# Optimization experiments

Measured on AMD Instinct MI355X. Metric: run time of the kernel, lower is better.

Reference implementation:

```python
import jax, jax.numpy as jnp
import numpy as np
import math

N_HEAD = 16

def _rope_tables(seq, dh, dtype):
    inv_freq = 1.0 / (10000.0 ** (jnp.arange(0, dh, 2, dtype=jnp.float32) / dh))
    angle = jnp.arange(seq, dtype=jnp.float32)[:, None] * inv_freq[None, :]  # [S, dh/2]
    sin = jnp.repeat(jnp.sin(angle), 2, axis=-1).astype(dtype)  # [S, dh]
    cos = jnp.repeat(jnp.cos(angle), 2, axis=-1).astype(dtype)
    return sin, cos

def _rotate_half(x):
    x_even = x[..., ::2]
    x_odd = x[..., 1::2]
    return jnp.stack([-x_odd, x_even], axis=-1).reshape(x.shape)

def _apply_rope(x, sin, cos):
    # x: [B, H, S, dh]; sin/cos: [S, dh]
    return x * cos[None, None] + _rotate_half(x) * sin[None, None]

def setup_inputs() -> dict:
    key = jax.random.key(0)
    ks = jax.random.split(key, 9)
    B, S, D = 2, 2048, 2048
    scale = 1.0 / math.sqrt(D)
    x = jax.random.normal(ks[0], (B, S, D), dtype=jnp.float32)
    wq = jax.random.normal(ks[1], (D, D), dtype=jnp.float32) * scale
    wk = jax.random.normal(ks[2], (D, D), dtype=jnp.float32) * scale
    wv = jax.random.normal(ks[3], (D, D), dtype=jnp.float32) * scale
    wo = jax.random.normal(ks[4], (D, D), dtype=jnp.float32) * scale
    bq = jnp.zeros((D,), jnp.float32)
    bk = jnp.zeros((D,), jnp.float32)
    bv = jnp.zeros((D,), jnp.float32)
    bo = jnp.zeros((D,), jnp.float32)
    # causal mask: True = masked (strict upper triangle)
    mask = jnp.triu(jnp.ones((S, S), dtype=bool), k=1)[None, None]  # [1,1,S,S]
    return {"x": x, "wq": wq, "bq": bq, "wk": wk, "bk": bk, "wv": wv, "bv": bv,
            "wo": wo, "bo": bo, "mask": mask}

def reference(x, wq, bq, wk, bk, wv, bv, wo, bo, mask):
    B, S, D = x.shape
    H = N_HEAD
    dh = D // H
    # projections (torch Linear: x @ W.T + b)
    q = (x @ wq.T + bq).reshape(B, S, H, dh).transpose(0, 2, 1, 3)  # [B,H,S,dh]
    k = (x @ wk.T + bk).reshape(B, S, H, dh).transpose(0, 2, 1, 3)
    v = (x @ wv.T + bv).reshape(B, S, H, dh).transpose(0, 2, 1, 3)
    sin, cos = _rope_tables(S, dh, x.dtype)
    q = _apply_rope(q, sin, cos)
    k = _apply_rope(k, sin, cos)
    scores = jnp.einsum('bhqd,bhkd->bhqk', q, k) / math.sqrt(dh)
    scores = jnp.where(mask, -jnp.inf, scores)
    attn = jax.nn.softmax(scores, axis=-1)
    attn = jnp.nan_to_num(attn, nan=0.0)
    out = jnp.einsum('bhqk,bhkd->bhqd', attn, v)  # [B,H,S,dh]
    out = out.transpose(0, 2, 1, 3).reshape(B, S, D)
    return out @ wo.T + bo
```

## Files before the change

### kernel.cpp

```cpp
#include <hip/hip_runtime.h>
#include <math.h>


typedef _Float16 half8 __attribute__((ext_vector_type(8)));
typedef _Float16 half4v __attribute__((ext_vector_type(4)));
typedef float f32x4 __attribute__((ext_vector_type(4)));

__device__ __forceinline__ void gl_lds16(const void* g, void* l) {
  __builtin_amdgcn_global_load_lds(
      (const __attribute__((address_space(1))) unsigned int*)g,
      (__attribute__((address_space(3))) unsigned int*)l, 16, 0, 0);
}

__global__ void cast_f32_f16(const float* __restrict__ src, _Float16* __restrict__ dst, int n4) {
  int i = blockIdx.x * blockDim.x + threadIdx.x;
  if (i >= n4) return;
  float4 v = reinterpret_cast<const float4*>(src)[i];
  half4v o;
  o[0] = (_Float16)v.x; o[1] = (_Float16)v.y; o[2] = (_Float16)v.z; o[3] = (_Float16)v.w;
  reinterpret_cast<half4v*>(dst)[i] = o;
}

__global__ void cast_w(const float* __restrict__ w0, const float* __restrict__ w1,
                       const float* __restrict__ w2, const float* __restrict__ w3,
                       _Float16* __restrict__ wdst) {
  const float* s = blockIdx.y == 0 ? w0 : blockIdx.y == 1 ? w1 : blockIdx.y == 2 ? w2 : w3;
  int i = blockIdx.x * blockDim.x + threadIdx.x;
  float4 v = reinterpret_cast<const float4*>(s)[i];
  half4v o;
  o[0] = (_Float16)v.x; o[1] = (_Float16)v.y; o[2] = (_Float16)v.z; o[3] = (_Float16)v.w;
  reinterpret_cast<half4v*>(wdst)[(size_t)blockIdx.y * 1048576 + i] = o;
}

template <bool OUT_F32>
__global__ __launch_bounds__(512, 2) void gemm_bt256(
    const _Float16* __restrict__ A,
    const _Float16* __restrict__ B,
    const float* __restrict__ b0, const float* __restrict__ b1,
    const float* __restrict__ b2,
    void* __restrict__ Cout,
    int M, int N, int K) {
  __shared__ _Float16 As[2][16384];
  __shared__ _Float16 Bs[2][16384];
  const int bm = blockIdx.y * 256, bn = blockIdx.x * 256;
  const int tid = threadIdx.x;
  const int wave = tid >> 6, lane = tid & 63;
  const int quad = lane >> 4, l16 = lane & 15;
  const int wm = (wave >> 2) * 128, wn = (wave & 3) * 64;

  const int srow = tid >> 3;
  const int sslot = (tid & 7) ^ (srow & 7);
  const _Float16* Ag = A + (size_t)(bm + srow) * K + sslot * 8;
  const _Float16* Bg = B + (size_t)(bn + srow) * K + sslot * 8;

#define STAGE_A(buf, h, c, kt)                                      \
  gl_lds16(Ag + (size_t)((h) * 128 + (c) * 64) * K + (kt) * 64,     \
           &As[buf][(h) * 8192 + (c) * 4096 + tid * 8])
#define STAGE_B(buf, h, c, kt)                                      \
  gl_lds16(Bg + (size_t)((h) * 128 + (c) * 64) * K + (kt) * 64,     \
           &Bs[buf][(h) * 8192 + (c) * 4096 + tid * 8])

  const int axor = l16 & 7;
  const int sl0 = ((0 + quad) ^ axor) * 8;
  const int sl1 = ((4 + quad) ^ axor) * 8;
  const int aoff = (wm + l16) * 64;
  const int boff = (wn + l16) * 64;

#define RD_A(i, kk) \
  (*reinterpret_cast<const half8*>(&As[cur][aoff + (i) * 1024 + ((kk) ? sl1 : sl0)]))
#define RD_B(j, kk) \
  (*reinterpret_cast<const half8*>(&Bs[cur][boff + (j) * 1024 + ((kk) ? sl1 : sl0)]))

  f32x4 acc[8][4];
#pragma unroll
  for (int i = 0; i < 8; ++i)
#pragma unroll
    for (int j = 0; j < 4; ++j) acc[i][j] = f32x4{0.f, 0.f, 0.f, 0.f};

  half8 a[4][2], b[4][2];
  const int NT = K >> 6;

  STAGE_A(0, 0, 0, 0); STAGE_A(0, 0, 1, 0);
  STAGE_A(0, 1, 0, 0); STAGE_A(0, 1, 1, 0);
  STAGE_B(0, 0, 0, 0); STAGE_B(0, 0, 1, 0);
  STAGE_B(0, 1, 0, 0); STAGE_B(0, 1, 1, 0);
  if (NT > 1) {
    STAGE_A(1, 0, 0, 1); STAGE_A(1, 0, 1, 1);
    asm volatile("s_waitcnt vmcnt(2)");
  } else {
    asm volatile("s_waitcnt vmcnt(0)");
  }
  __builtin_amdgcn_s_barrier();

  for (int t = 0; t < NT; ++t) {
    const int cur = t & 1, nxt = cur ^ 1;
    const bool pf = (t + 1 < NT);
    const bool pf2 = (t + 2 < NT);

#pragma unroll
    for (int i = 0; i < 4; ++i) {
      a[i][0] = RD_A(i, 0); a[i][1] = RD_A(i, 1);
    }
#pragma unroll
    for (int j = 0; j < 2; ++j) {
      b[j][0] = RD_B(j, 0); b[j][1] = RD_B(j, 1);
    }
    if (pf) { STAGE_A(nxt, 1, 0, t + 1); STAGE_A(nxt, 1, 1, t + 1); }
    __builtin_amdgcn_s_barrier();
    __builtin_amdgcn_s_setprio(1);
#pragma unroll
    for (int i = 0; i < 4; ++i)
#pragma unroll
      for (int j = 0; j < 2; ++j) {
        acc[i][j] = __builtin_amdgcn_mfma_f32_16x16x32_f16(a[i][0], b[j][0], acc[i][j], 0, 0, 0);
        acc[i][j] = __builtin_amdgcn_mfma_f32_16x16x32_f16(a[i][1], b[j][1], acc[i][j], 0, 0, 0);
      }
    __builtin_amdgcn_s_setprio(0);
    __builtin_amdgcn_s_barrier();

#pragma unroll
    for (int j = 2; j < 4; ++j) {
      b[j][0] = RD_B(j, 0); b[j][1] = RD_B(j, 1);
    }
    if (pf) { STAGE_B(nxt, 0, 0, t + 1); STAGE_B(nxt, 0, 1, t + 1); }
    __builtin_amdgcn_s_barrier();
    __builtin_amdgcn_s_setprio(1);
#pragma unroll
    for (int i = 0; i < 4; ++i)
#pragma unroll
      for (int j = 2; j < 4; ++j) {
        acc[i][j] = __builtin_amdgcn_mfma_f32_16x16x32_f16(a[i][0], b[j][0], acc[i][j], 0, 0, 0);
        acc[i][j] = __builtin_amdgcn_mfma_f32_16x16x32_f16(a[i][1], b[j][1], acc[i][j], 0, 0, 0);
      }
    __builtin_amdgcn_s_setprio(0);
    __builtin_amdgcn_s_barrier();

#pragma unroll
    for (int i = 0; i < 4; ++i) {
      a[i][0] = RD_A(i + 4, 0); a[i][1] = RD_A(i + 4, 1);
    }
    if (pf) { STAGE_B(nxt, 1, 0, t + 1); STAGE_B(nxt, 1, 1, t + 1); }
    __builtin_amdgcn_s_barrier();
    __builtin_amdgcn_s_setprio(1);
#pragma unroll
    for (int i = 0; i < 4; ++i)
#pragma unroll
      for (int j = 0; j < 2; ++j) {
        acc[i + 4][j] = __builtin_amdgcn_mfma_f32_16x16x32_f16(a[i][0], b[j][0], acc[i + 4][j], 0, 0, 0);
        acc[i + 4][j] = __builtin_amdgcn_mfma_f32_16x16x32_f16(a[i][1], b[j][1], acc[i + 4][j], 0, 0, 0);
      }
    __builtin_amdgcn_s_setprio(0);
    __builtin_amdgcn_s_barrier();

    if (pf2) { STAGE_A(cur, 0, 0, t + 2); STAGE_A(cur, 0, 1, t + 2); }
    __builtin_amdgcn_s_barrier();
    __builtin_amdgcn_s_setprio(1);
#pragma unroll
    for (int i = 0; i < 4; ++i)
#pragma unroll
      for (int j = 2; j < 4; ++j) {
        acc[i + 4][j] = __builtin_amdgcn_mfma_f32_16x16x32_f16(a[i][0], b[j][0], acc[i + 4][j], 0, 0, 0);
        acc[i + 4][j] = __builtin_amdgcn_mfma_f32_16x16x32_f16(a[i][1], b[j][1], acc[i + 4][j], 0, 0, 0);
      }
    __builtin_amdgcn_s_setprio(0);
    if (pf2)
      asm volatile("s_waitcnt vmcnt(2)");
    else
      asm volatile("s_waitcnt vmcnt(0)");
    __builtin_amdgcn_s_barrier();
  }

#pragma unroll
  for (int j = 0; j < 4; ++j) {
    const int gc = bn + wn + j * 16 + l16;
    const float* bp = (gc < 2048) ? b0 : (gc < 4096 ? b1 : b2);
    const float bz = bp[gc & 2047];
#pragma unroll
    for (int i = 0; i < 8; ++i) {
#pragma unroll
      for (int r = 0; r < 4; ++r) {
        const int gr = bm + wm + i * 16 + quad * 4 + r;
        float v = acc[i][j][r] + bz;
        if (OUT_F32)
          reinterpret_cast<float*>(Cout)[(size_t)gr * N + gc] = v;
        else
          reinterpret_cast<_Float16*>(Cout)[(size_t)gr * N + gc] = (_Float16)v;
      }
    }
  }
#undef STAGE_A
#undef STAGE_B
#undef RD_A
#undef RD_B
}

__global__ void rope_inplace(_Float16* __restrict__ qkv, int ngroups) {
  int idx = blockIdx.x * blockDim.x + threadIdx.x;
  if (idx >= ngroups) return;
  int m = idx >> 8;
  int g = idx & 255;
  int s = m & 2047;
  const float scale = 0.088388347648318447f;
  size_t base = (size_t)m * 6144 + g * 8;
  half8 qv = *reinterpret_cast<const half8*>(qkv + base);
  half8 kv = *reinterpret_cast<const half8*>(qkv + base + 2048);
  half8 qo, ko;
#pragma unroll
  for (int j = 0; j < 4; ++j) {
    int i = (g * 4 + j) & 63;
    float ang = (float)s * exp2f(-0.2076205059304601f * (float)i);
    float sn, cs;
    __sincosf(ang, &sn, &cs);
    float e = (float)qv[j * 2], o = (float)qv[j * 2 + 1];
    qo[j * 2]     = (_Float16)((e * cs - o * sn) * scale);
    qo[j * 2 + 1] = (_Float16)((o * cs + e * sn) * scale);
    e = (float)kv[j * 2]; o = (float)kv[j * 2 + 1];
    ko[j * 2]     = (_Float16)(e * cs - o * sn);
    ko[j * 2 + 1] = (_Float16)(o * cs + e * sn);
  }
  *reinterpret_cast<half8*>(qkv + base) = qo;
  *reinterpret_cast<half8*>(qkv + base + 2048) = ko;
}

__global__ __launch_bounds__(256) void transpose_v(const _Float16* __restrict__ qkv,
                                                   _Float16* __restrict__ vt) {
  __shared__ _Float16 t[64][72];
  const int s0 = blockIdx.x * 64;
  const int d0 = blockIdx.y * 64;
  const int bh = blockIdx.z;
  const int b = bh >> 4, h = bh & 15;
  const int tid = threadIdx.x;
#pragma unroll
  for (int p = 0; p < 2; ++p) {
    int chunk = p * 256 + tid;
    int r = chunk >> 3, c8 = (chunk & 7) * 8;
    *reinterpret_cast<half8*>(&t[r][c8]) = *reinterpret_cast<const half8*>(
        &qkv[(size_t)(b * 2048 + s0 + r) * 6144 + 4096 + h * 128 + d0 + c8]);
  }
  __syncthreads();
#pragma unroll
  for (int p = 0; p < 2; ++p) {
    int chunk = p * 256 + tid;
    int dr = chunk >> 3, c8 = (chunk & 7) * 8;
    half8 o;
#pragma unroll
    for (int j = 0; j < 8; ++j) o[j] = t[c8 + j][dr];
    *reinterpret_cast<half8*>(&vt[(size_t)(bh * 128 + d0 + dr) * 2048 + s0 + c8]) = o;
  }
}

__global__ __launch_bounds__(256, 2) void attn_kernel(
    const _Float16* __restrict__ QKV,
    const _Float16* __restrict__ VT,
    _Float16* __restrict__ ctx) {
  constexpr int LD = 6144, S = 2048;
  __shared__ _Float16 Ks[2][8192];
  __shared__ _Float16 Vs[2][8192];
  __shared__ _Float16 P[4][16][80];
  const int bid = blockIdx.x;
  const int bh = bid & 31;
  const int qt = 31 - (bid >> 5);
  const int b = bh >> 4, h = bh & 15;
  const int tid = threadIdx.x;
  const int wv = tid >> 6, lane = tid & 63;
  const int quad = lane >> 4, l16 = lane & 15;
  const int q0 = qt * 64 + wv * 16;

  const _Float16* qp = QKV + (size_t)(b * S + q0 + l16) * LD + h * 128;
  half8 aq[4];
#pragma unroll
  for (int ks = 0; ks < 4; ++ks)
    aq[ks] = *reinterpret_cast<const half8*>(qp + ks * 32 + quad * 8);

  const _Float16* gk[4];
  const _Float16* gv[4];
  int lofs[4];
#pragma unroll
  for (int p = 0; p < 4; ++p) {
    int c = p * 256 + tid;
    int cl16 = c & 15, cqd = (c >> 4) & 3;
    int cks = (c >> 6) & 3, cf = c >> 8;
    gk[p] = QKV + (size_t)(b * S + cf * 16 + cl16) * LD + 2048 + h * 128 + cks * 32 + cqd * 8;
    int ckv = (c >> 6) & 1, ct = c >> 7;
    gv[p] = VT + (size_t)(bh * 128 + ct * 16 + cl16) * S + ckv * 32 + cqd * 8;
    lofs[p] = c * 8;
  }

  f32x4 acc[8];
#pragma unroll
  for (int t = 0; t < 8; ++t) acc[t] = f32x4{0.f, 0.f, 0.f, 0.f};
  f32x4 lacc = f32x4{0.f, 0.f, 0.f, 0.f};
  float m_i[4];
#pragma unroll
  for (int r = 0; r < 4; ++r) m_i[r] = -INFINITY;

  half8 ones;
#pragma unroll
  for (int j = 0; j < 8; ++j) ones[j] = (_Float16)1.0f;

#pragma unroll
  for (int p = 0; p < 4; ++p) gl_lds16(gk[p], &Ks[0][lofs[p]]);
#pragma unroll
  for (int p = 0; p < 4; ++p) gl_lds16(gv[p], &Vs[0][lofs[p]]);

  for (int j = 0; j <= qt; ++j) {
    __syncthreads();
    const int cur = j & 1;
    if (j < qt) {
      const size_t ko = (size_t)(j + 1) * 64 * LD;
      const int vo = (j + 1) * 64;
#pragma unroll
      for (int p = 0; p < 4; ++p) gl_lds16(gk[p] + ko, &Ks[cur ^ 1][lofs[p]]);
#pragma unroll
      for (int p = 0; p < 4; ++p) gl_lds16(gv[p] + vo, &Vs[cur ^ 1][lofs[p]]);
    }
    f32x4 sf[4];
#pragma unroll
    for (int f = 0; f < 4; ++f) sf[f] = f32x4{0.f, 0.f, 0.f, 0.f};
#pragma unroll
    for (int f = 0; f < 4; ++f)
#pragma unroll
      for (int ks = 0; ks < 4; ++ks) {
        half8 bk = *reinterpret_cast<const half8*>(&Ks[cur][((f * 4 + ks) * 4 + quad) * 128 + l16 * 8]);
        sf[f] = __builtin_amdgcn_mfma_f32_16x16x32_f16(aq[ks], bk, sf[f], 0, 0, 0);
      }
    if (j == qt) {
      const int key0 = j * 64;
#pragma unroll
      for (int f = 0; f < 4; ++f) {
        const int key = key0 + f * 16 + l16;
#pragma unroll
        for (int r = 0; r < 4; ++r) {
          const int row = q0 + quad * 4 + r;
          sf[f][r] = (key <= row) ? sf[f][r] : -1e30f;
        }
      }
    }
    float alpha[4];
#pragma unroll
    for (int r = 0; r < 4; ++r) {
      float tm = fmaxf(fmaxf(sf[0][r], sf[1][r]), fmaxf(sf[2][r], sf[3][r]));
      tm = fmaxf(tm, __shfl_xor(tm, 1));
      tm = fmaxf(tm, __shfl_xor(tm, 2));
      tm = fmaxf(tm, __shfl_xor(tm, 4));
      tm = fmaxf(tm, __shfl_xor(tm, 8));
      const float mn = fmaxf(m_i[r], tm);
      alpha[r] = __expf(m_i[r] - mn);
      m_i[r] = mn;
    }
#pragma unroll
    for (int f = 0; f < 4; ++f)
#pragma unroll
      for (int r = 0; r < 4; ++r)
        P[wv][quad * 4 + r][f * 16 + l16] = (_Float16)__expf(sf[f][r] - m_i[r]);
    half8 pa0 = *reinterpret_cast<const half8*>(&P[wv][l16][quad * 8]);
    half8 pa1 = *reinterpret_cast<const half8*>(&P[wv][l16][32 + quad * 8]);
#pragma unroll
    for (int t = 0; t < 8; ++t)
#pragma unroll
      for (int r = 0; r < 4; ++r) acc[t][r] *= alpha[r];
#pragma unroll
    for (int r = 0; r < 4; ++r) lacc[r] *= alpha[r];
#pragma unroll
    for (int t = 0; t < 8; ++t) {
      half8 bv0 = *reinterpret_cast<const half8*>(&Vs[cur][((t * 2 + 0) * 4 + quad) * 128 + l16 * 8]);
      half8 bv1 = *reinterpret_cast<const half8*>(&Vs[cur][((t * 2 + 1) * 4 + quad) * 128 + l16 * 8]);
      acc[t] = __builtin_amdgcn_mfma_f32_16x16x32_f16(pa0, bv0, acc[t], 0, 0, 0);
      acc[t] = __builtin_amdgcn_mfma_f32_16x16x32_f16(pa1, bv1, acc[t], 0, 0, 0);
    }
    lacc = __builtin_amdgcn_mfma_f32_16x16x32_f16(pa0, ones, lacc, 0, 0, 0);
    lacc = __builtin_amdgcn_mfma_f32_16x16x32_f16(pa1, ones, lacc, 0, 0, 0);
  }

  float inv[4];
#pragma unroll
  for (int r = 0; r < 4; ++r) inv[r] = 1.0f / lacc[r];
#pragma unroll
  for (int t = 0; t < 8; ++t)
#pragma unroll
    for (int r = 0; r < 4; ++r)
      ctx[(size_t)(b * S + q0 + quad * 4 + r) * 2048 + h * 128 + t * 16 + l16] =
          (_Float16)(acc[t][r] * inv[r]);
}

extern "C" void kernel_launch(void* const* d_in, const int* in_sizes, int n_in,
                              void* d_out, int out_size, void* d_ws, size_t ws_size,
                              hipStream_t stream) {
  const float* x  = (const float*)d_in[0];
  const float* wq = (const float*)d_in[1];
  const float* bq = (const float*)d_in[2];
  const float* wk = (const float*)d_in[3];
  const float* bk = (const float*)d_in[4];
  const float* wv = (const float*)d_in[5];
  const float* bv = (const float*)d_in[6];
  const float* wo = (const float*)d_in[7];
  const float* bo = (const float*)d_in[8];

  _Float16* W      = (_Float16*)d_ws;
  _Float16* xh     = W;
  _Float16* wqkvh  = xh + 8388608;
  _Float16* woh    = wqkvh + 12582912;
  _Float16* qkvlin = woh + 4194304;
  _Float16* vT     = xh;
  _Float16* ctx    = wqkvh;

  cast_f32_f16<<<8192, 256, 0, stream>>>(x, xh, 2097152);
  cast_w<<<dim3(4096, 4), 256, 0, stream>>>(wq, wk, wv, wo, wqkvh);

  gemm_bt256<false><<<dim3(24, 16), 512, 0, stream>>>(xh, wqkvh, bq, bk, bv, qkvlin,
                                                      4096, 6144, 2048);

  rope_inplace<<<4096, 256, 0, stream>>>(qkvlin, 1048576);
  transpose_v<<<dim3(32, 2, 32), 256, 0, stream>>>(qkvlin, vT);
  attn_kernel<<<1024, 256, 0, stream>>>(qkvlin, vT, ctx);

  gemm_bt256<true><<<dim3(8, 16), 512, 0, stream>>>(ctx, woh, bo, bo, bo, (float*)d_out,
                                                    4096, 2048, 2048);
}
```

Baseline: 452.9 us.

## Reorder GEMM staging so B and half of A prefetch two tiles ahead

Changes the LDS layout of the B tile so that each 64-row staging chunk holds the rows needed by one phase across all wave columns. This lets B chunks and the first A half be issued two K-tiles ahead into the current buffer as soon as they are consumed, rather than one tile ahead. The vmcnt waits are raised to keep more loads in flight, with the aim of hiding global-load latency better. The cost is more complex row remapping and tighter correctness conditions on when LDS regions are overwritten.

```diff
diff --git a/kernel.cpp b/kernel.cpp
--- a/kernel.cpp
+++ b/kernel.cpp
@@ -49,27 +49,31 @@
   const int wm = (wave >> 2) * 128, wn = (wave & 3) * 64;
 
   const int srow = tid >> 3;
-  const int sslot = (tid & 7) ^ (srow & 7);
-  const _Float16* Ag = A + (size_t)(bm + srow) * K + sslot * 8;
-  const _Float16* Bg = B + (size_t)(bn + srow) * K + sslot * 8;
-
-#define STAGE_A(buf, h, c, kt)                                      \
-  gl_lds16(Ag + (size_t)((h) * 128 + (c) * 64) * K + (kt) * 64,     \
-           &As[buf][(h) * 8192 + (c) * 4096 + tid * 8])
-#define STAGE_B(buf, h, c, kt)                                      \
-  gl_lds16(Bg + (size_t)((h) * 128 + (c) * 64) * K + (kt) * 64,     \
-           &Bs[buf][(h) * 8192 + (c) * 4096 + tid * 8])
+  const int sx = (tid & 7) ^ (srow & 7);
+  const _Float16* Ag = A + (size_t)(bm + srow) * K + sx * 8;
+  const _Float16* Bg[4];
+#pragma unroll
+  for (int c = 0; c < 4; ++c) {
+    int r = (((c * 2 + (srow >> 5)) & 3) << 6) + ((c >> 1) << 5) + (srow & 31);
+    Bg[c] = B + (size_t)(bn + r) * K + sx * 8;
+  }
+
+#define STAGE_A(buf, R, kt) \
+  gl_lds16(Ag + (size_t)(R) * K + (kt) * 64, &As[buf][(R) * 64 + tid * 8])
+#define STAGE_B(buf, c, kt) \
+  gl_lds16(Bg[c] + (kt) * 64, &Bs[buf][(c) * 4096 + tid * 8])
 
   const int axor = l16 & 7;
   const int sl0 = ((0 + quad) ^ axor) * 8;
   const int sl1 = ((4 + quad) ^ axor) * 8;
   const int aoff = (wm + l16) * 64;
-  const int boff = (wn + l16) * 64;
+  const int q4 = (wn >> 6) * 32;
 
 #define RD_A(i, kk) \
   (*reinterpret_cast<const half8*>(&As[cur][aoff + (i) * 1024 + ((kk) ? sl1 : sl0)]))
 #define RD_B(j, kk) \
-  (*reinterpret_cast<const half8*>(&Bs[cur][boff + (j) * 1024 + ((kk) ? sl1 : sl0)]))
+  (*reinterpret_cast<const half8*>( \
+      &Bs[cur][((((j) >> 1) * 128 + q4 + ((j) & 1) * 16 + l16)) * 64 + ((kk) ? sl1 : sl0)]))
 
   f32x4 acc[8][4];
 #pragma unroll
@@ -80,13 +84,15 @@
   half8 a[4][2], b[4][2];
   const int NT = K >> 6;
 
-  STAGE_A(0, 0, 0, 0); STAGE_A(0, 0, 1, 0);
-  STAGE_A(0, 1, 0, 0); STAGE_A(0, 1, 1, 0);
-  STAGE_B(0, 0, 0, 0); STAGE_B(0, 0, 1, 0);
-  STAGE_B(0, 1, 0, 0); STAGE_B(0, 1, 1, 0);
+  STAGE_A(0, 0, 0); STAGE_A(0, 128, 0);
+  STAGE_B(0, 0, 0); STAGE_B(0, 1, 0);
+  STAGE_B(0, 2, 0); STAGE_B(0, 3, 0);
+  STAGE_A(0, 64, 0); STAGE_A(0, 192, 0);
   if (NT > 1) {
-    STAGE_A(1, 0, 0, 1); STAGE_A(1, 0, 1, 1);
-    asm volatile("s_waitcnt vmcnt(2)");
+    STAGE_A(1, 0, 1); STAGE_A(1, 128, 1);
+    STAGE_B(1, 0, 1); STAGE_B(1, 1, 1);
+    STAGE_B(1, 2, 1); STAGE_B(1, 3, 1);
+    asm volatile("s_waitcnt vmcnt(6)");
   } else {
     asm volatile("s_waitcnt vmcnt(0)");
   }
@@ -94,7 +100,7 @@
 
   for (int t = 0; t < NT; ++t) {
     const int cur = t & 1, nxt = cur ^ 1;
-    const bool pf = (t + 1 < NT);
+    const bool pf1 = (t + 1 < NT);
     const bool pf2 = (t + 2 < NT);
 
 #pragma unroll
@@ -105,7 +111,7 @@
     for (int j = 0; j < 2; ++j) {
       b[j][0] = RD_B(j, 0); b[j][1] = RD_B(j, 1);
     }
-    if (pf) { STAGE_A(nxt, 1, 0, t + 1); STAGE_A(nxt, 1, 1, t + 1); }
+    if (pf1) { STAGE_A(nxt, 64, t + 1); STAGE_A(nxt, 192, t + 1); }
     __builtin_amdgcn_s_barrier();
     __builtin_amdgcn_s_setprio(1);
 #pragma unroll
@@ -122,7 +128,7 @@
     for (int j = 2; j < 4; ++j) {
       b[j][0] = RD_B(j, 0); b[j][1] = RD_B(j, 1);
     }
-    if (pf) { STAGE_B(nxt, 0, 0, t + 1); STAGE_B(nxt, 0, 1, t + 1); }
+    if (pf2) { STAGE_A(cur, 0, t + 2); STAGE_A(cur, 128, t + 2); }
     __builtin_amdgcn_s_barrier();
     __builtin_amdgcn_s_setprio(1);
 #pragma unroll
@@ -139,7 +145,7 @@
     for (int i = 0; i < 4; ++i) {
       a[i][0] = RD_A(i + 4, 0); a[i][1] = RD_A(i + 4, 1);
     }
-    if (pf) { STAGE_B(nxt, 1, 0, t + 1); STAGE_B(nxt, 1, 1, t + 1); }
+    if (pf2) { STAGE_B(cur, 0, t + 2); STAGE_B(cur, 1, t + 2); }
     __builtin_amdgcn_s_barrier();
     __builtin_amdgcn_s_setprio(1);
 #pragma unroll
@@ -152,7 +158,7 @@
     __builtin_amdgcn_s_setprio(0);
     __builtin_amdgcn_s_barrier();
 
-    if (pf2) { STAGE_A(cur, 0, 0, t + 2); STAGE_A(cur, 0, 1, t + 2); }
+    if (pf2) { STAGE_B(cur, 2, t + 2); STAGE_B(cur, 3, t + 2); }
     __builtin_amdgcn_s_barrier();
     __builtin_amdgcn_s_setprio(1);
 #pragma unroll
@@ -164,7 +170,7 @@
       }
     __builtin_amdgcn_s_setprio(0);
     if (pf2)
-      asm volatile("s_waitcnt vmcnt(2)");
+      asm volatile("s_waitcnt vmcnt(6)");
     else
       asm volatile("s_waitcnt vmcnt(0)");
     __builtin_amdgcn_s_barrier();
```

Measured after the change: 451.6 us. No clear change (-0.3%).
